# Kernel optimization log

Hardware: AMD Instinct MI355X
Metric: run time of the kernel (lower is better)

Reference implementation:

```python
import jax, jax.numpy as jnp
import numpy as np
from jax import lax


def affine_grid(theta, H, W):
    # theta [2,3]; torch F.affine_grid, align_corners=False (pixel centers)
    xs = (jnp.arange(W, dtype=jnp.float32) * 2 + 1) / W - 1
    ys = (jnp.arange(H, dtype=jnp.float32) * 2 + 1) / H - 1
    gx, gy = jnp.meshgrid(xs, ys)  # [H,W]
    base = jnp.stack([gx, gy, jnp.ones_like(gx)], -1)  # [H,W,3]
    return jnp.einsum('hwk,jk->hwj', base, theta)  # [H,W,2]


def grid_sample(img, grid):
    # img [C,H,W], grid [H,W,2] normalized; bilinear, zero padding, align_corners=False
    C, H, W = img.shape
    x = ((grid[..., 0] + 1) * W - 1) * 0.5
    y = ((grid[..., 1] + 1) * H - 1) * 0.5
    x0 = jnp.floor(x); y0 = jnp.floor(y)
    x1 = x0 + 1; y1 = y0 + 1
    wx1 = x - x0; wx0 = 1 - wx1
    wy1 = y - y0; wy0 = 1 - wy1
    def gather(xi, yi):
        xic = jnp.clip(xi, 0, W - 1).astype(jnp.int32)
        yic = jnp.clip(yi, 0, H - 1).astype(jnp.int32)
        valid = ((xi >= 0) & (xi <= W - 1) & (yi >= 0) & (yi <= H - 1)).astype(img.dtype)
        return img[:, yic, xic] * valid  # [C,H,W]
    return (gather(x0, y0) * (wx0 * wy0) + gather(x1, y0) * (wx1 * wy0)
            + gather(x0, y1) * (wx0 * wy1) + gather(x1, y1) * (wx1 * wy1))


def warp_one(feat, t):
    # feat [C,H,W], t [4,4]: rotate then translate, two bilinear resamples (as in source)
    C, H, W = feat.shape
    zero = jnp.zeros((), feat.dtype); one = jnp.ones((), feat.dtype)
    theta_rot = jnp.stack([jnp.stack([t[0, 0], t[0, 1], zero]),
                           jnp.stack([t[1, 0], t[1, 1], zero])])
    x_tr = 4 * t[0, 3] / 128
    y_tr = -(4 * t[1, 3]) / 128
    theta_tr = jnp.stack([jnp.stack([one, zero, x_tr]),
                          jnp.stack([zero, one, y_tr])])
    f = grid_sample(feat, affine_grid(theta_rot, H, W))
    return grid_sample(f, affine_grid(theta_tr, H, W))


def conv2d(x, w, b):
    y = lax.conv_general_dilated(x, w, (1, 1), 'SAME',
                                 dimension_numbers=('NCHW', 'OIHW', 'NCHW'))
    return y + b[None, :, None, None]


def convgru_step0(x, wx, wh, bx, bh):
    # single-layer ConvGRU, one timestep, h0 = 0 => hidden convs vanish, only bh remains
    C = wh.shape[1]
    gx = conv2d(x, wx, bx)  # [N,3C,H,W]
    xr, xz, xn = jnp.split(gx, 3, axis=1)
    br, bz, bn = jnp.split(bh, 3)
    r = jax.nn.sigmoid(xr + br[None, :, None, None])
    z = jax.nn.sigmoid(xz + bz[None, :, None, None])
    n = jnp.tanh(xn + r * bn[None, :, None, None])
    return (1 - z) * n  # h' = (1-z)*n + z*0


def setup_inputs() -> dict:
    key = jax.random.key(0)
    ks = jax.random.split(key, 6)
    B, A, C, H, W = 2, 5, 64, 128, 128
    feats = jax.random.normal(ks[0], (B, A, C, H, W), jnp.float32)
    ang = jax.random.uniform(ks[1], (B, A, A), minval=-np.pi, maxval=np.pi).astype(jnp.float32)
    ca, sa = jnp.cos(ang), jnp.sin(ang)
    t = jnp.zeros((B, A, A, 4, 4), jnp.float32)
    t = t.at[..., 0, 0].set(ca).at[..., 0, 1].set(-sa)
    t = t.at[..., 1, 0].set(sa).at[..., 1, 1].set(ca)
    tr = jax.random.uniform(ks[2], (B, A, A, 2), minval=-10.0, maxval=10.0)
    t = t.at[..., 0, 3].set(tr[..., 0]).at[..., 1, 3].set(tr[..., 1])
    wx = jax.random.normal(ks[3], (3 * C, 2 * C, 3, 3), jnp.float32) * 0.05
    wh = jax.random.normal(ks[4], (3 * C, C, 3, 3), jnp.float32) * 0.05
    bx = jnp.zeros((3 * C,), jnp.float32)
    bh = jnp.zeros((3 * C,), jnp.float32)
    return {'feats': feats, 'trans': t, 'wx': wx, 'wh': wh, 'bx': bx, 'bh': bh,
            'num_agent': A, 'gnn_iter': 2}


def reference(feats, trans, wx, wh, bx, bh, num_agent, gnn_iter):
    trans = lax.stop_gradient(trans)  # source builds theta via torch.tensor (detached)
    B, A, C, H, W = feats.shape
    mask = 1.0 - jnp.eye(A, dtype=feats.dtype)  # exclude self (j != i)
    warp = jax.vmap(jax.vmap(jax.vmap(warp_one, (0, 0)), (None, 0)), (0, 0))
    for _ in range(gnn_iter):
        warped = warp(feats, trans)  # [B, A_i, A_j, C, H, W]
        mean = jnp.einsum('bijchw,ij->bichw', warped, mask) / (A - 1)
        cat = jnp.concatenate([feats, mean], axis=2).reshape(B * A, 2 * C, H, W)
        feats = convgru_step0(cat, wx, wh, bx, bh).reshape(B, A, C, H, W)
    return feats
```

## Files before the change

kernel.cpp:

```cpp
#include <hip/hip_runtime.h>
#include <cmath>

#define BB 2
#define AA 5
#define CH 64
#define HH 128
#define WW 128
#define HW (HH*WW)
#define NIMG (BB*AA)

typedef __attribute__((ext_vector_type(8))) _Float16 half8;
typedef __attribute__((ext_vector_type(4))) float floatx4;

__device__ inline half8 hzero() {
    half8 v;
#pragma unroll
    for (int e = 0; e < 8; ++e) v[e] = (_Float16)0.f;
    return v;
}

__device__ inline float fsigmoid(float x) {
    return __builtin_amdgcn_rcpf(1.f + __builtin_amdgcn_exp2f(-1.442695041f * x));
}
__device__ inline float ftanh(float x) {
    return 2.f * fsigmoid(2.f * x) - 1.f;
}

__global__ __launch_bounds__(256) void to_nhwc_kernel(
    const float* __restrict__ src, _Float16* __restrict__ dst)
{
    const int img = blockIdx.y;
    const int cg  = blockIdx.x & 7;
    const int pb  = blockIdx.x >> 3;
    const int p   = pb * 256 + threadIdx.x;
    const float* s = src + ((size_t)img * CH + cg * 8) * HW + p;
    half8 v;
#pragma unroll
    for (int e = 0; e < 8; ++e) v[e] = (_Float16)s[e * HW];
    *(half8*)(dst + ((size_t)img * HW + p) * 128 + cg * 8) = v;
}

__global__ __launch_bounds__(256) void pack_w_kernel(
    const float* __restrict__ wx, half8* __restrict__ wp)
{
    int idx = blockIdx.x * 256 + threadIdx.x;
    if (idx >= 4 * 9 * 4 * 192) return;
    int oc = idx % 192; int r = idx / 192;
    int gk = r & 3; r >>= 2; int tap = r % 9; int cc = r / 9;
    int ky = tap / 3, kx = tap % 3;
    half8 v;
#pragma unroll
    for (int e = 0; e < 8; ++e)
        v[e] = (_Float16)wx[(((size_t)oc * 128 + cc * 32 + gk * 8 + e) * 3 + ky) * 3 + kx];
    wp[idx] = v;
}

__global__ __launch_bounds__(256) void warp_mean_kernel(
    const _Float16* __restrict__ nh,
    const float* __restrict__ trans,
    _Float16* __restrict__ nhw)
{
    __shared__ float f_lds[16][17][18];

    const int tile = blockIdx.x;
    const int tx0 = (tile & 7) * 16;
    const int ty0 = (tile >> 3) * 16;
    const int c0  = blockIdx.y * 16;
    const int bi  = blockIdx.z;
    const int b   = bi / AA, i = bi % AA;
    const int tid = threadIdx.x;
    const int ltx = tid & 15, lty = tid >> 4;

    float acc[16];
#pragma unroll
    for (int c = 0; c < 16; ++c) acc[c] = 0.f;

    for (int j = 0; j < AA; ++j) {
        if (j == i) continue;
        const float* t = trans + (((size_t)b * AA + i) * AA + j) * 16;
        const float t00 = t[0], t01 = t[1], t03 = t[3];
        const float t10 = t[4], t11 = t[5], t13 = t[7];
        const float dxs = 2.f * t03;
        const float dys = -2.f * t13;
        const float sxf = floorf(dxs), syf = floorf(dys);
        const int sx = (int)sxf, sy = (int)syf;
        const float fx = dxs - sxf, fy = dys - syf;
        const _Float16* srcj = nh + (size_t)(b * AA + j) * HW * 128 + c0;

        for (int idx = tid; idx < 17 * 17; idx += 256) {
            const int lx = idx % 17, ly = idx / 17;
            const int qx = tx0 + sx + lx;
            const int qy = ty0 + sy + ly;
            const bool qin = (qx >= 0) & (qx < WW) & (qy >= 0) & (qy < HH);
            if (!qin) {
#pragma unroll
                for (int c = 0; c < 16; ++c) f_lds[c][ly][lx] = 0.f;
            } else {
                const float xn = (2 * qx + 1) * (1.0f / WW) - 1.f;
                const float yn = (2 * qy + 1) * (1.0f / HH) - 1.f;
                const float sxn = t00 * xn + t01 * yn;
                const float syn = t10 * xn + t11 * yn;
                const float px = 64.f * sxn + 63.5f;
                const float py = 64.f * syn + 63.5f;
                const float x0f = floorf(px), y0f = floorf(py);
                const int x0 = (int)x0f, y0 = (int)y0f;
                const float wx1 = px - x0f, wx0 = 1.f - wx1;
                const float wy1 = py - y0f, wy0 = 1.f - wy1;
                const bool vx0 = (x0 >= 0) & (x0 < WW);
                const bool vx1 = (x0 + 1 >= 0) & (x0 + 1 < WW);
                const bool vy0 = (y0 >= 0) & (y0 < HH);
                const bool vy1 = (y0 + 1 >= 0) & (y0 + 1 < HH);
                const int cx0 = min(max(x0, 0), WW - 1);
                const int cx1 = min(max(x0 + 1, 0), WW - 1);
                const int cy0 = min(max(y0, 0), HH - 1);
                const int cy1 = min(max(y0 + 1, 0), HH - 1);
                const float w00 = (vx0 & vy0) ? wx0 * wy0 : 0.f;
                const float w01 = (vx1 & vy0) ? wx1 * wy0 : 0.f;
                const float w10 = (vx0 & vy1) ? wx0 * wy1 : 0.f;
                const float w11 = (vx1 & vy1) ? wx1 * wy1 : 0.f;
                const size_t o00 = ((size_t)cy0 * WW + cx0) * 128;
                const size_t o01 = ((size_t)cy0 * WW + cx1) * 128;
                const size_t o10 = ((size_t)cy1 * WW + cx0) * 128;
                const size_t o11 = ((size_t)cy1 * WW + cx1) * 128;
                const half8 a0 = *(const half8*)(srcj + o00);
                const half8 a1 = *(const half8*)(srcj + o00 + 8);
                const half8 b0 = *(const half8*)(srcj + o01);
                const half8 b1 = *(const half8*)(srcj + o01 + 8);
                const half8 c0v = *(const half8*)(srcj + o10);
                const half8 c1v = *(const half8*)(srcj + o10 + 8);
                const half8 d0 = *(const half8*)(srcj + o11);
                const half8 d1 = *(const half8*)(srcj + o11 + 8);
#pragma unroll
                for (int c = 0; c < 16; ++c) {
                    const float p00 = (c < 8) ? (float)a0[c & 7] : (float)a1[c & 7];
                    const float p01 = (c < 8) ? (float)b0[c & 7] : (float)b1[c & 7];
                    const float p10 = (c < 8) ? (float)c0v[c & 7] : (float)c1v[c & 7];
                    const float p11 = (c < 8) ? (float)d0[c & 7] : (float)d1[c & 7];
                    f_lds[c][ly][lx] = w00 * p00 + w01 * p01 + w10 * p10 + w11 * p11;
                }
            }
        }
        __syncthreads();

        const float wA = (1.f - fx) * (1.f - fy);
        const float wB = fx * (1.f - fy);
        const float wC = (1.f - fx) * fy;
        const float wD = fx * fy;
#pragma unroll
        for (int c = 0; c < 16; ++c) {
            const float v00 = f_lds[c][lty][ltx];
            const float v01 = f_lds[c][lty][ltx + 1];
            const float v10 = f_lds[c][lty + 1][ltx];
            const float v11 = f_lds[c][lty + 1][ltx + 1];
            acc[c] += wA * v00 + wB * v01 + wC * v10 + wD * v11;
        }
        __syncthreads();
    }

    const float inv = 1.f / (AA - 1);
    _Float16* dst = nhw + ((size_t)bi * HW + (ty0 + lty) * WW + tx0 + ltx) * 128 + 64 + c0;
    half8 o0, o1;
#pragma unroll
    for (int c = 0; c < 8; ++c) { o0[c] = (_Float16)(acc[c] * inv); o1[c] = (_Float16)(acc[c + 8] * inv); }
    *(half8*)dst = o0;
    *(half8*)(dst + 8) = o1;
}

__global__ __launch_bounds__(256, 4) void conv_gru_mfma(
    const _Float16* __restrict__ in,
    const half8* __restrict__ wp,
    const float* __restrict__ bx,
    const float* __restrict__ bh,
    float* __restrict__ out_f32,
    _Float16* __restrict__ out_f16)
{
    __shared__ half8 lds_in[16 * 6 * 18];

    const int tid = threadIdx.x;
    const int img = blockIdx.z;
    const int x0 = (blockIdx.x & 7) * 16;
    const int y0 = (blockIdx.x >> 3) * 4;
    const int w   = tid >> 6;
    const int ln  = tid & 15;
    const int kq  = (tid & 63) >> 4;

    const _Float16* inimg = in + (size_t)img * HW * 128;
    for (int f = tid; f < 1728; f += 256) {
        const int g = f / 108; const int r = f % 108;
        const int row = r / 18; const int col = r % 18;
        const int y = y0 + row - 1, x = x0 + col - 1;
        half8 v = hzero();
        if ((unsigned)x < (unsigned)WW && (unsigned)y < (unsigned)HH)
            v = *(const half8*)(inimg + ((size_t)y * WW + x) * 128 + g * 8);
        lds_in[f] = v;
    }

    floatx4 acc[4][3];
#pragma unroll
    for (int s = 0; s < 4; ++s)
#pragma unroll
        for (int t = 0; t < 3; ++t)
#pragma unroll
            for (int r = 0; r < 4; ++r) acc[s][t][r] = 0.f;

    __syncthreads();

    const half8* wbase = wp + kq * 192 + w * 16 + ln;
    half8 bnx[3];
#pragma unroll
    for (int t = 0; t < 3; ++t) bnx[t] = wbase[t * 64];

#pragma unroll
    for (int s = 0; s < 36; ++s) {
        const int cc = s / 9, tap = s - cc * 9;
        const int dy = tap / 3, dx = tap - dy * 3;
        half8 bcur[3];
#pragma unroll
        for (int t = 0; t < 3; ++t) bcur[t] = bnx[t];
        if (s + 1 < 36) {
            const half8* wsrc = wbase + (size_t)(s + 1) * 768;
#pragma unroll
            for (int t = 0; t < 3; ++t) bnx[t] = wsrc[t * 64];
        }
        half8 a[4];
#pragma unroll
        for (int t = 0; t < 4; ++t)
            a[t] = lds_in[((cc * 4 + kq) * 6 + t + dy) * 18 + ln + dx];
#pragma unroll
        for (int t = 0; t < 4; ++t)
#pragma unroll
            for (int u = 0; u < 3; ++u)
                acc[t][u] = __builtin_amdgcn_mfma_f32_16x16x32_f16(a[t], bcur[u], acc[t][u], 0, 0, 0);
    }

    const int c = w * 16 + ln;
    const float bxr = bx[c] + bh[c];
    const float bxz = bx[64 + c] + bh[64 + c];
    const float bxn = bx[128 + c];
    const float bnn = bh[128 + c];
#pragma unroll
    for (int s = 0; s < 4; ++s) {
        const int y = y0 + s;
#pragma unroll
        for (int reg = 0; reg < 4; ++reg) {
            const int x = x0 + kq * 4 + reg;
            const float xr = acc[s][0][reg] + bxr;
            const float xz = acc[s][1][reg] + bxz;
            const float xn = acc[s][2][reg] + bxn;
            const float rg = fsigmoid(xr);
            const float zg = fsigmoid(xz);
            const float n  = ftanh(xn + rg * bnn);
            const float h  = (1.f - zg) * n;
            if (out_f32)
                out_f32[((size_t)img * CH + c) * HW + y * WW + x] = h;
            else
                out_f16[((size_t)img * HW + y * WW + x) * 128 + c] = (_Float16)h;
        }
    }
}

extern "C" void kernel_launch(void* const* d_in, const int* in_sizes, int n_in,
                              void* d_out, int out_size, void* d_ws, size_t ws_size,
                              hipStream_t stream) {
    const float* feats = (const float*)d_in[0];
    const float* trans = (const float*)d_in[1];
    const float* wx    = (const float*)d_in[2];
    const float* bx    = (const float*)d_in[4];
    const float* bh    = (const float*)d_in[5];
    float* out = (float*)d_out;

    char* ws = (char*)d_ws;
    half8*    wpack = (half8*)ws;
    _Float16* B1 = (_Float16*)(ws + 442368);
    _Float16* B2 = (_Float16*)(ws + 442368 + (size_t)NIMG * HW * 128 * 2);

    pack_w_kernel<<<108, 256, 0, stream>>>(wx, wpack);
    to_nhwc_kernel<<<dim3(512, NIMG), 256, 0, stream>>>(feats, B1);

    dim3 wgrid(64, 4, NIMG);
    dim3 cgrid(256, 1, NIMG);

    warp_mean_kernel<<<wgrid, 256, 0, stream>>>(B1, trans, B1);
    conv_gru_mfma<<<cgrid, 256, 0, stream>>>(B1, wpack, bx, bh, nullptr, B2);
    warp_mean_kernel<<<wgrid, 256, 0, stream>>>(B2, trans, B2);
    conv_gru_mfma<<<cgrid, 256, 0, stream>>>(B2, wpack, bx, bh, out, nullptr);
}
```

Measured before the change: 371.8 us.

## Restructure warp-mean to all-channel tiles with fp16 LDS and enlarge conv tile

Each warp-mean block now handles a 16x8 pixel tile across all 64 channels instead of 16x16 pixels by 16 channels. Each thread computes the first rotation resample for 8 channels of one point with a single half8 load per corner, stores the result packed as fp16 pairs in LDS, and does the translation resample with packed half2 math. This should cut duplicated coordinate math, issue fewer and wider gathers, and shrink LDS use. The conv-GRU kernel doubles its row tile to 8, giving each wave more MFMAs per weight load, with lower occupancy bounds. The cost is reduced accumulation precision in fp16 and higher register pressure in the conv kernel.

```diff
diff --git a/kernel.cpp b/kernel.cpp
--- a/kernel.cpp
+++ b/kernel.cpp
@@ -10,7 +10,10 @@
 #define NIMG (BB*AA)
 
 typedef __attribute__((ext_vector_type(8))) _Float16 half8;
+typedef __attribute__((ext_vector_type(2))) _Float16 half2v;
 typedef __attribute__((ext_vector_type(4))) float floatx4;
+typedef unsigned int uint32;
+typedef __attribute__((ext_vector_type(4))) uint32 uint4v;
 
 __device__ inline half8 hzero() {
     half8 v;
@@ -55,25 +58,29 @@
     wp[idx] = v;
 }
 
-__global__ __launch_bounds__(256) void warp_mean_kernel(
+__global__ __launch_bounds__(256, 5) void warp_mean_kernel(
     const _Float16* __restrict__ nh,
     const float* __restrict__ trans,
     _Float16* __restrict__ nhw)
 {
-    __shared__ float f_lds[16][17][18];
+    __shared__ uint32 f_lds[32 * 9 * 18];
 
     const int tile = blockIdx.x;
     const int tx0 = (tile & 7) * 16;
-    const int ty0 = (tile >> 3) * 16;
-    const int c0  = blockIdx.y * 16;
+    const int ty0 = (tile >> 3) * 8;
     const int bi  = blockIdx.z;
     const int b   = bi / AA, i = bi % AA;
     const int tid = threadIdx.x;
-    const int ltx = tid & 15, lty = tid >> 4;
-
-    float acc[16];
-#pragma unroll
-    for (int c = 0; c < 16; ++c) acc[c] = 0.f;
+
+    const int slc = tid & 7;
+    const int ptb = tid >> 3;
+    const int col = tid & 15;
+    const int row = (tid >> 4) & 7;
+    const int chh = tid >> 7;
+
+    half2v acc[16];
+#pragma unroll
+    for (int c = 0; c < 16; ++c) acc[c] = (half2v)(_Float16)0.f;
 
     for (int j = 0; j < AA; ++j) {
         if (j == i) continue;
@@ -85,88 +92,94 @@
         const float sxf = floorf(dxs), syf = floorf(dys);
         const int sx = (int)sxf, sy = (int)syf;
         const float fx = dxs - sxf, fy = dys - syf;
-        const _Float16* srcj = nh + (size_t)(b * AA + j) * HW * 128 + c0;
-
-        for (int idx = tid; idx < 17 * 17; idx += 256) {
-            const int lx = idx % 17, ly = idx / 17;
-            const int qx = tx0 + sx + lx;
-            const int qy = ty0 + sy + ly;
-            const bool qin = (qx >= 0) & (qx < WW) & (qy >= 0) & (qy < HH);
-            if (!qin) {
-#pragma unroll
-                for (int c = 0; c < 16; ++c) f_lds[c][ly][lx] = 0.f;
-            } else {
-                const float xn = (2 * qx + 1) * (1.0f / WW) - 1.f;
-                const float yn = (2 * qy + 1) * (1.0f / HH) - 1.f;
-                const float sxn = t00 * xn + t01 * yn;
-                const float syn = t10 * xn + t11 * yn;
-                const float px = 64.f * sxn + 63.5f;
-                const float py = 64.f * syn + 63.5f;
-                const float x0f = floorf(px), y0f = floorf(py);
-                const int x0 = (int)x0f, y0 = (int)y0f;
-                const float wx1 = px - x0f, wx0 = 1.f - wx1;
-                const float wy1 = py - y0f, wy0 = 1.f - wy1;
-                const bool vx0 = (x0 >= 0) & (x0 < WW);
-                const bool vx1 = (x0 + 1 >= 0) & (x0 + 1 < WW);
-                const bool vy0 = (y0 >= 0) & (y0 < HH);
-                const bool vy1 = (y0 + 1 >= 0) & (y0 + 1 < HH);
-                const int cx0 = min(max(x0, 0), WW - 1);
-                const int cx1 = min(max(x0 + 1, 0), WW - 1);
-                const int cy0 = min(max(y0, 0), HH - 1);
-                const int cy1 = min(max(y0 + 1, 0), HH - 1);
-                const float w00 = (vx0 & vy0) ? wx0 * wy0 : 0.f;
-                const float w01 = (vx1 & vy0) ? wx1 * wy0 : 0.f;
-                const float w10 = (vx0 & vy1) ? wx0 * wy1 : 0.f;
-                const float w11 = (vx1 & vy1) ? wx1 * wy1 : 0.f;
-                const size_t o00 = ((size_t)cy0 * WW + cx0) * 128;
-                const size_t o01 = ((size_t)cy0 * WW + cx1) * 128;
-                const size_t o10 = ((size_t)cy1 * WW + cx0) * 128;
-                const size_t o11 = ((size_t)cy1 * WW + cx1) * 128;
-                const half8 a0 = *(const half8*)(srcj + o00);
-                const half8 a1 = *(const half8*)(srcj + o00 + 8);
-                const half8 b0 = *(const half8*)(srcj + o01);
-                const half8 b1 = *(const half8*)(srcj + o01 + 8);
-                const half8 c0v = *(const half8*)(srcj + o10);
-                const half8 c1v = *(const half8*)(srcj + o10 + 8);
-                const half8 d0 = *(const half8*)(srcj + o11);
-                const half8 d1 = *(const half8*)(srcj + o11 + 8);
-#pragma unroll
-                for (int c = 0; c < 16; ++c) {
-                    const float p00 = (c < 8) ? (float)a0[c & 7] : (float)a1[c & 7];
-                    const float p01 = (c < 8) ? (float)b0[c & 7] : (float)b1[c & 7];
-                    const float p10 = (c < 8) ? (float)c0v[c & 7] : (float)c1v[c & 7];
-                    const float p11 = (c < 8) ? (float)d0[c & 7] : (float)d1[c & 7];
-                    f_lds[c][ly][lx] = w00 * p00 + w01 * p01 + w10 * p10 + w11 * p11;
+        const _Float16* srcj = nh + (size_t)(b * AA + j) * HW * 128 + slc * 8;
+
+        __syncthreads();
+#pragma unroll
+        for (int it = 0; it < 5; ++it) {
+            const int pt = it * 32 + ptb;
+            if (pt < 153) {
+                const int prow = pt / 17;
+                const int pcol = pt - prow * 17;
+                const int qx = tx0 + sx + pcol;
+                const int qy = ty0 + sy + prow;
+                float e[8];
+#pragma unroll
+                for (int k = 0; k < 8; ++k) e[k] = 0.f;
+                if (((unsigned)qx < (unsigned)WW) & ((unsigned)qy < (unsigned)HH)) {
+                    const float xn = (2 * qx + 1) * (1.0f / WW) - 1.f;
+                    const float yn = (2 * qy + 1) * (1.0f / HH) - 1.f;
+                    const float px = 64.f * (t00 * xn + t01 * yn) + 63.5f;
+                    const float py = 64.f * (t10 * xn + t11 * yn) + 63.5f;
+                    const float x0f = floorf(px), y0f = floorf(py);
+                    const int x0 = (int)x0f, y0 = (int)y0f;
+                    const float wx1 = px - x0f, wx0 = 1.f - wx1;
+                    const float wy1 = py - y0f, wy0 = 1.f - wy1;
+                    const bool vx0 = (x0 >= 0) & (x0 < WW);
+                    const bool vx1 = (x0 + 1 >= 0) & (x0 + 1 < WW);
+                    const bool vy0 = (y0 >= 0) & (y0 < HH);
+                    const bool vy1 = (y0 + 1 >= 0) & (y0 + 1 < HH);
+                    const int cx0 = min(max(x0, 0), WW - 1);
+                    const int cx1 = min(max(x0 + 1, 0), WW - 1);
+                    const int cy0 = min(max(y0, 0), HH - 1);
+                    const int cy1 = min(max(y0 + 1, 0), HH - 1);
+                    const float w00 = (vx0 & vy0) ? wx0 * wy0 : 0.f;
+                    const float w01 = (vx1 & vy0) ? wx1 * wy0 : 0.f;
+                    const float w10 = (vx0 & vy1) ? wx0 * wy1 : 0.f;
+                    const float w11 = (vx1 & vy1) ? wx1 * wy1 : 0.f;
+                    const half8 A = *(const half8*)(srcj + ((size_t)cy0 * WW + cx0) * 128);
+                    const half8 Bv = *(const half8*)(srcj + ((size_t)cy0 * WW + cx1) * 128);
+                    const half8 Cv = *(const half8*)(srcj + ((size_t)cy1 * WW + cx0) * 128);
+                    const half8 D = *(const half8*)(srcj + ((size_t)cy1 * WW + cx1) * 128);
+#pragma unroll
+                    for (int k = 0; k < 8; ++k)
+                        e[k] = w00 * (float)A[k] + w01 * (float)Bv[k]
+                             + w10 * (float)Cv[k] + w11 * (float)D[k];
+                }
+                const int lb = slc * 4 * 162 + prow * 18 + pcol;
+#pragma unroll
+                for (int k = 0; k < 4; ++k) {
+                    half2v p;
+                    p[0] = (_Float16)e[2 * k];
+                    p[1] = (_Float16)e[2 * k + 1];
+                    f_lds[lb + k * 162] = __builtin_bit_cast(uint32, p);
                 }
             }
         }
         __syncthreads();
 
-        const float wA = (1.f - fx) * (1.f - fy);
-        const float wB = fx * (1.f - fy);
-        const float wC = (1.f - fx) * fy;
-        const float wD = fx * fy;
+        const float wAf = (1.f - fx) * (1.f - fy);
+        const float wBf = fx * (1.f - fy);
+        const float wCf = (1.f - fx) * fy;
+        const float wDf = fx * fy;
+        half2v wA2 = (half2v)(_Float16)wAf;
+        half2v wB2 = (half2v)(_Float16)wBf;
+        half2v wC2 = (half2v)(_Float16)wCf;
+        half2v wD2 = (half2v)(_Float16)wDf;
+        const uint32* fp0 = f_lds + (chh * 16) * 162 + row * 18 + col;
 #pragma unroll
         for (int c = 0; c < 16; ++c) {
-            const float v00 = f_lds[c][lty][ltx];
-            const float v01 = f_lds[c][lty][ltx + 1];
-            const float v10 = f_lds[c][lty + 1][ltx];
-            const float v11 = f_lds[c][lty + 1][ltx + 1];
-            acc[c] += wA * v00 + wB * v01 + wC * v10 + wD * v11;
+            const uint32* fp = fp0 + c * 162;
+            const half2v v00 = __builtin_bit_cast(half2v, fp[0]);
+            const half2v v01 = __builtin_bit_cast(half2v, fp[1]);
+            const half2v v10 = __builtin_bit_cast(half2v, fp[18]);
+            const half2v v11 = __builtin_bit_cast(half2v, fp[19]);
+            acc[c] += v00 * wA2 + v01 * wB2 + v10 * wC2 + v11 * wD2;
         }
-        __syncthreads();
     }
 
-    const float inv = 1.f / (AA - 1);
-    _Float16* dst = nhw + ((size_t)bi * HW + (ty0 + lty) * WW + tx0 + ltx) * 128 + 64 + c0;
-    half8 o0, o1;
-#pragma unroll
-    for (int c = 0; c < 8; ++c) { o0[c] = (_Float16)(acc[c] * inv); o1[c] = (_Float16)(acc[c + 8] * inv); }
-    *(half8*)dst = o0;
-    *(half8*)(dst + 8) = o1;
-}
-
-__global__ __launch_bounds__(256, 4) void conv_gru_mfma(
+    const half2v q = (half2v)(_Float16)0.25f;
+    uint32 os[16];
+#pragma unroll
+    for (int c = 0; c < 16; ++c) os[c] = __builtin_bit_cast(uint32, acc[c] * q);
+    uint4v* dst = (uint4v*)(nhw + ((size_t)bi * HW + (ty0 + row) * WW + tx0 + col) * 128
+                            + 64 + chh * 32);
+#pragma unroll
+    for (int k = 0; k < 4; ++k)
+        dst[k] = (uint4v){os[4 * k], os[4 * k + 1], os[4 * k + 2], os[4 * k + 3]};
+}
+
+__global__ __launch_bounds__(256, 3) void conv_gru_mfma(
     const _Float16* __restrict__ in,
     const half8* __restrict__ wp,
     const float* __restrict__ bx,
@@ -174,30 +187,30 @@
     float* __restrict__ out_f32,
     _Float16* __restrict__ out_f16)
 {
-    __shared__ half8 lds_in[16 * 6 * 18];
+    __shared__ half8 lds_in[16 * 10 * 18];
 
     const int tid = threadIdx.x;
     const int img = blockIdx.z;
     const int x0 = (blockIdx.x & 7) * 16;
-    const int y0 = (blockIdx.x >> 3) * 4;
+    const int y0 = (blockIdx.x >> 3) * 8;
     const int w   = tid >> 6;
     const int ln  = tid & 15;
     const int kq  = (tid & 63) >> 4;
 
     const _Float16* inimg = in + (size_t)img * HW * 128;
-    for (int f = tid; f < 1728; f += 256) {
-        const int g = f / 108; const int r = f % 108;
-        const int row = r / 18; const int col = r % 18;
-        const int y = y0 + row - 1, x = x0 + col - 1;
+    for (int f = tid; f < 2880; f += 256) {
+        const int g = f / 180; const int r = f % 180;
+        const int prow = r / 18; const int pcol = r % 18;
+        const int y = y0 + prow - 1, x = x0 + pcol - 1;
         half8 v = hzero();
         if ((unsigned)x < (unsigned)WW && (unsigned)y < (unsigned)HH)
             v = *(const half8*)(inimg + ((size_t)y * WW + x) * 128 + g * 8);
         lds_in[f] = v;
     }
 
-    floatx4 acc[4][3];
-#pragma unroll
-    for (int s = 0; s < 4; ++s)
+    floatx4 acc[8][3];
+#pragma unroll
+    for (int s = 0; s < 8; ++s)
 #pragma unroll
         for (int t = 0; t < 3; ++t)
 #pragma unroll
@@ -214,6 +227,7 @@
     for (int s = 0; s < 36; ++s) {
         const int cc = s / 9, tap = s - cc * 9;
         const int dy = tap / 3, dx = tap - dy * 3;
+        half2v dummy;
         half8 bcur[3];
 #pragma unroll
         for (int t = 0; t < 3; ++t) bcur[t] = bnx[t];
@@ -222,12 +236,12 @@
 #pragma unroll
             for (int t = 0; t < 3; ++t) bnx[t] = wsrc[t * 64];
         }
-        half8 a[4];
-#pragma unroll
-        for (int t = 0; t < 4; ++t)
-            a[t] = lds_in[((cc * 4 + kq) * 6 + t + dy) * 18 + ln + dx];
-#pragma unroll
-        for (int t = 0; t < 4; ++t)
+        half8 a[8];
+#pragma unroll
+        for (int t = 0; t < 8; ++t)
+            a[t] = lds_in[((cc * 4 + kq) * 10 + t + dy) * 18 + ln + dx];
+#pragma unroll
+        for (int t = 0; t < 8; ++t)
 #pragma unroll
             for (int u = 0; u < 3; ++u)
                 acc[t][u] = __builtin_amdgcn_mfma_f32_16x16x32_f16(a[t], bcur[u], acc[t][u], 0, 0, 0);
@@ -239,7 +253,7 @@
     const float bxn = bx[128 + c];
     const float bnn = bh[128 + c];
 #pragma unroll
-    for (int s = 0; s < 4; ++s) {
+    for (int s = 0; s < 8; ++s) {
         const int y = y0 + s;
 #pragma unroll
         for (int reg = 0; reg < 4; ++reg) {
@@ -277,8 +291,8 @@
     pack_w_kernel<<<108, 256, 0, stream>>>(wx, wpack);
     to_nhwc_kernel<<<dim3(512, NIMG), 256, 0, stream>>>(feats, B1);
 
-    dim3 wgrid(64, 4, NIMG);
-    dim3 cgrid(256, 1, NIMG);
+    dim3 wgrid(128, 1, NIMG);
+    dim3 cgrid(128, 1, NIMG);
 
     warp_mean_kernel<<<wgrid, 256, 0, stream>>>(B1, trans, B1);
     conv_gru_mfma<<<cgrid, 256, 0, stream>>>(B1, wpack, bx, bh, nullptr, B2);
```

Measured after the change: 629.6 us. +69.3%, slower.
